# Kernel optimization log

Hardware: AMD Instinct MI355X
Metric: run time of the kernel (lower is better)

The kernel has to match this reference:

```python
import jax, jax.numpy as jnp
import numpy as np


def _conv3x3(x, w):
    # NCHW input, OIHW weight, stride 1, padding 1 (SAME for 3x3)
    return jax.lax.conv_general_dilated(
        x, w, window_strides=(1, 1), padding=((1, 1), (1, 1)),
        dimension_numbers=('NCHW', 'OIHW', 'NCHW'))


def _conv1x1(x, w):
    return jax.lax.conv_general_dilated(
        x, w, window_strides=(1, 1), padding=((0, 0), (0, 0)),
        dimension_numbers=('NCHW', 'OIHW', 'NCHW'))


def setup_inputs() -> dict:
    key = jax.random.key(0)
    k_x, k_w1, k_w2, k_wm = jax.random.split(key, 4)
    N, C, H, W = 16, 256, 64, 64
    fan = C * 9
    x = jax.random.normal(k_x, (N, C, H, W), dtype=jnp.float32)
    w1 = jax.random.normal(k_w1, (C, C, 3, 3), dtype=jnp.float32) * (2.0 / fan) ** 0.5
    w2 = jax.random.normal(k_w2, (C, C, 3, 3), dtype=jnp.float32) * (2.0 / fan) ** 0.5
    w_mask = jax.random.normal(k_wm, (1, C, 1, 1), dtype=jnp.float32) * (1.0 / C) ** 0.5
    b_mask = jnp.zeros((1,), dtype=jnp.float32)
    return {'x': x, 'w1': w1, 'w2': w2, 'w_mask': w_mask, 'b_mask': b_mask}


def reference(x, w1, w2, w_mask, b_mask):
    # MaskUnit: 1x1 conv -> logits -> hard binary mask (straight-through estimator)
    logits = _conv1x1(x, w_mask) + b_mask[None, :, None, None]  # [N,1,H,W]
    hard = (logits > 0).astype(x.dtype)
    mask = logits + jax.lax.stop_gradient(hard - logits)        # std mask, binary in fwd
    # dilated mask: 3x3 max-pool (covers 3x3 receptive field of active outputs)
    mask_dilate = jax.lax.reduce_window(
        mask, -jnp.inf, jax.lax.max, (1, 1, 3, 3), (1, 1, 1, 1), 'SAME')
    # sparse branch: conv1 gated by dilated mask, conv2 gated by std mask
    h = jax.nn.relu(_conv3x3(x, w1) * mask_dilate)
    h = jax.nn.relu(_conv3x3(h, w2) * mask)
    # apply_mask + residual (mask binary -> h*mask == h already, kept for fidelity)
    out = x + h * mask
    return out
```

## Files before the change

kernel.cpp:

```cpp
#include <hip/hip_runtime.h>
#include <hip/hip_bf16.h>

#define C_ 256
#define H_ 64
#define W_ 64
#define N_ 16
#define HW_ 4096
#define IMG_ (C_ * HW_)
#define PADIMG_ (66 * 66 * 256)
#define WT_ELEMS_ (9 * 16 * 256 * 16)

typedef short bf16x8 __attribute__((ext_vector_type(8)));
typedef float f32x16 __attribute__((ext_vector_type(16)));

__device__ __forceinline__ unsigned short f2bf(float f) {
  __hip_bfloat16 h = __float2bfloat16(f);
  return *reinterpret_cast<unsigned short*>(&h);
}

__device__ __forceinline__ void gld_lds16(const void* g, void* l) {
  __builtin_amdgcn_global_load_lds(
      (const __attribute__((address_space(1))) void*)g,
      (__attribute__((address_space(3))) void*)l, 16, 0, 0);
}

__global__ __launch_bounds__(256) void xpadmask_kernel(
    const float* __restrict__ x, const float* __restrict__ wm,
    const float* __restrict__ bm, short* __restrict__ Xp,
    unsigned char* __restrict__ mask) {
  __shared__ unsigned short lds[64 * 260];
  __shared__ float wms[256];
  __shared__ double sums[4][64];
  const int h = blockIdx.x, img = blockIdx.y;
  const int tid = threadIdx.x;
  const int wv = tid >> 6, wl = tid & 63;
  wms[tid] = wm[tid];
  __syncthreads();
  const float* xi = x + (size_t)img * IMG_ + h * 64;
  double a0 = 0.0, a1 = 0.0, a2 = 0.0, a3 = 0.0;
#pragma unroll 4
  for (int i = 0; i < 16; ++i) {
#pragma unroll
    for (int u = 0; u < 4; ++u) {
      int c = (i * 4 + u) * 4 + wv;
      float v = xi[(size_t)c * HW_ + wl];
      lds[wl * 260 + c] = f2bf(v);
      double p = (double)v * (double)wms[c];
      if (u == 0) a0 += p;
      else if (u == 1) a1 += p;
      else if (u == 2) a2 += p;
      else a3 += p;
    }
  }
  sums[wv][wl] = (a0 + a1) + (a2 + a3);
  __syncthreads();
  short* Xpi = Xp + (size_t)img * PADIMG_ + ((h + 1) * 66 + 1) * 256;
#pragma unroll
  for (int j = 0; j < 16; ++j) {
    int w = j * 4 + wv;
    int c4 = wl * 4;
    uint2 d = *(const uint2*)&lds[w * 260 + c4];
    *(uint2*)&Xpi[(size_t)w * 256 + c4] = d;
  }
  if (wv == 0) {
    double t = sums[0][wl] + sums[1][wl] + sums[2][wl] + sums[3][wl] +
               (double)bm[0];
    mask[img * HW_ + h * 64 + wl] = (t > 0.0) ? 1 : 0;
  }
}

__global__ __launch_bounds__(256) void wt_kernel(
    const float* __restrict__ w1, const float* __restrict__ w2,
    short* __restrict__ Wt1, short* __restrict__ Wt2) {
  const int k = blockIdx.x, c = threadIdx.x;
  const float* src = blockIdx.y ? w2 : w1;
  short* dst = blockIdx.y ? Wt2 : Wt1;
  const float* s = src + ((size_t)k * 256 + c) * 9;
  const int kc = c >> 4, ce = c & 15;
#pragma unroll
  for (int t = 0; t < 9; ++t)
    dst[(((size_t)t * 16 + kc) * 256 + k) * 16 + ce] = (short)f2bf(s[t]);
}

__global__ __launch_bounds__(128) void halo_zero(short* __restrict__ Xp,
                                                 short* __restrict__ Hp) {
  int p = blockIdx.x;
  int r, c;
  if (p < 66) { r = 0; c = p; }
  else if (p < 132) { r = 65; c = p - 66; }
  else if (p < 196) { r = p - 131; c = 0; }
  else { r = p - 195; c = 65; }
  short* buf = blockIdx.z ? Hp : Xp;
  unsigned int* d = (unsigned int*)(buf + (size_t)blockIdx.y * PADIMG_ +
                                    (size_t)(r * 66 + c) * 256);
  d[threadIdx.x] = 0u;
}

#define BBUF 10560

__device__ __forceinline__ void stage_B(short* sm, int buf, const short* Xb,
                                        int ko, int wave, int lane) {
  short* Bd = sm + buf * BBUF;
#pragma unroll
  for (int q = 0; q < 3; ++q) {
    int n = wave + 8 * q;
    if (n > 21) n = 21;
    const int h = (n >= 11) ? 1 : 0;
    const int i = n - h * 11;
    const int row0 = (i < 10) ? i * 64 : 596;
    gld_lds16(Xb + (size_t)(row0 + lane) * 256 + ko + h * 8,
              Bd + h * 5280 + row0 * 8);
  }
}

template <int EPI>
__global__ __launch_bounds__(512, 4) void conv_mfma(
    const short* __restrict__ src, const short* __restrict__ Wt,
    const unsigned char* __restrict__ gate, const float* __restrict__ xres,
    short* __restrict__ dstH, float* __restrict__ dstF, int swz) {
  __shared__ __align__(16) short sm[3 * BBUF];

  const int tid = threadIdx.x;
  const int lane = tid & 63, wave = tid >> 6;
  const int ln31 = lane & 31, kh = lane >> 5;

  int bx, by, bz;
  {
    int d = blockIdx.x + 4 * (blockIdx.y + 8 * blockIdx.z);
    if (swz) {
      int k = d & 7, j = d >> 3;
      bx = j & 3;
      by = (j >> 2) & 7;
      bz = ((j >> 5) << 3) + k;
    } else {
      bx = blockIdx.x;
      by = blockIdx.y;
      bz = blockIdx.z;
    }
  }
  const int ch0 = bx * 64;
  const int h0 = by * 8;
  const int img = bz;

  const short* Xb = src + (size_t)img * PADIMG_ + (size_t)(h0 * 66) * 256;
  const short* WL = Wt + ((size_t)(ch0 + ln31)) * 16 + kh * 8;

  f32x16 acc[2][2];
#pragma unroll
  for (int i = 0; i < 2; ++i)
#pragma unroll
    for (int j = 0; j < 2; ++j)
#pragma unroll
      for (int e = 0; e < 16; ++e) acc[i][j][e] = 0.f;

  stage_B(sm, 0, Xb, 0, wave, lane);
  stage_B(sm, 1, Xb, 16, wave, lane);
  bf16x8 wc0 = *(const bf16x8*)(WL);
  bf16x8 wc1 = *(const bf16x8*)(WL + 512);
  asm volatile("s_waitcnt vmcnt(2)\n\ts_barrier" ::: "memory");

  int c0 = 0, c1 = 1, c2 = 2;
  for (int kk = 0; kk < 16; ++kk) {
    const short* Bth = sm + c0 * BBUF + kh * 5280 + (wave * 66 + ln31) * 8;
#pragma unroll
    for (int t = 0; t < 9; ++t) {
      const int ntkc = (t < 8) ? ((t + 1) * 16 + kk) : (kk + 1);
      bf16x8 na0 = *(const bf16x8*)(WL + (size_t)ntkc * 4096);
      bf16x8 na1 = *(const bf16x8*)(WL + (size_t)ntkc * 4096 + 512);
      const int dy = t / 3, dx = t % 3;
      bf16x8 b[2];
#pragma unroll
      for (int j = 0; j < 2; ++j)
        b[j] = *(const bf16x8*)(Bth + (dy * 66 + j * 32 + dx) * 8);
      __builtin_amdgcn_s_setprio(1);
#pragma unroll
      for (int j = 0; j < 2; ++j) {
        acc[0][j] = __builtin_amdgcn_mfma_f32_32x32x16_bf16(wc0, b[j],
                                                            acc[0][j], 0, 0, 0);
        acc[1][j] = __builtin_amdgcn_mfma_f32_32x32x16_bf16(wc1, b[j],
                                                            acc[1][j], 0, 0, 0);
      }
      __builtin_amdgcn_s_setprio(0);
      wc0 = na0;
      wc1 = na1;
    }
    if (kk < 14) stage_B(sm, c2, Xb, (kk + 2) * 16, wave, lane);
    if (kk < 15) asm volatile("s_barrier" ::: "memory");
    const int tmp = c0;
    c0 = c1;
    c1 = c2;
    c2 = tmp;
  }

  const int r = h0 + wave;
#pragma unroll
  for (int j = 0; j < 2; ++j) {
    const int col = j * 32 + ln31;
    const int pidx = r * 64 + col;
    unsigned int g;
    if (EPI == 0) {
      g = 0;
#pragma unroll
      for (int dy = -1; dy <= 1; ++dy) {
        const int rr = r + dy;
        if (rr < 0 || rr >= H_) continue;
#pragma unroll
        for (int dx = -1; dx <= 1; ++dx) {
          const int cc = col + dx;
          if (cc < 0 || cc >= W_) continue;
          g |= gate[img * HW_ + rr * W_ + cc];
        }
      }
    } else {
      g = gate[img * HW_ + pidx];
    }
#pragma unroll
    for (int i = 0; i < 2; ++i) {
      const f32x16 v = acc[i][j];
#pragma unroll
      for (int rg = 0; rg < 4; ++rg) {
        const int ch = ch0 + i * 32 + rg * 8 + kh * 4;
        float e0 = g ? fmaxf(v[rg * 4 + 0], 0.f) : 0.f;
        float e1 = g ? fmaxf(v[rg * 4 + 1], 0.f) : 0.f;
        float e2 = g ? fmaxf(v[rg * 4 + 2], 0.f) : 0.f;
        float e3 = g ? fmaxf(v[rg * 4 + 3], 0.f) : 0.f;
        if (EPI == 0) {
          uint2 u;
          u.x = (unsigned int)f2bf(e0) | ((unsigned int)f2bf(e1) << 16);
          u.y = (unsigned int)f2bf(e2) | ((unsigned int)f2bf(e3) << 16);
          short* dp = dstH + (size_t)img * PADIMG_ +
                      ((size_t)((r + 1) * 66 + (col + 1))) * 256 + ch;
          *(uint2*)dp = u;
        } else {
          size_t o = (size_t)img * IMG_ + (size_t)ch * HW_ + pidx;
          dstF[o] = xres[o] + e0;
          dstF[o + HW_] = xres[o + HW_] + e1;
          dstF[o + 2 * HW_] = xres[o + 2 * HW_] + e2;
          dstF[o + 3 * HW_] = xres[o + 3 * HW_] + e3;
        }
      }
    }
  }
}

extern "C" void kernel_launch(void* const* d_in, const int* in_sizes, int n_in,
                              void* d_out, int out_size, void* d_ws,
                              size_t ws_size, hipStream_t stream) {
  const float* x = (const float*)d_in[0];
  const float* w1 = (const float*)d_in[1];
  const float* w2 = (const float*)d_in[2];
  const float* wmask = (const float*)d_in[3];
  const float* bmask = (const float*)d_in[4];
  float* out = (float*)d_out;

  char* ws = (char*)d_ws;
  unsigned char* mask = (unsigned char*)ws;
  short* Wt1 = (short*)(ws + 65536);
  short* Wt2 = Wt1 + WT_ELEMS_;
  const size_t fixed = 65536 + 4 * (size_t)WT_ELEMS_;
  short* Xp = (short*)(ws + fixed);

  const size_t tailpad = 32768;
  const size_t per_img = 2 * (size_t)PADIMG_ * 2;
  int B = (ws_size > fixed + tailpad)
              ? (int)((ws_size - fixed - tailpad) / per_img) : 0;
  if (B > N_) B = N_;
  if (B < 1) B = 1;
  short* Hp = Xp + (size_t)B * PADIMG_;

  wt_kernel<<<dim3(256, 2), 256, 0, stream>>>(w1, w2, Wt1, Wt2);
  halo_zero<<<dim3(260, B, 2), 128, 0, stream>>>(Xp, Hp);

  for (int n0 = 0; n0 < N_; n0 += B) {
    const int nb = (N_ - n0 < B) ? (N_ - n0) : B;
    const int swz = (nb % 8 == 0) ? 1 : 0;
    xpadmask_kernel<<<dim3(64, nb), 256, 0, stream>>>(
        x + (size_t)n0 * IMG_, wmask, bmask, Xp, mask + n0 * HW_);
    conv_mfma<0><<<dim3(4, 8, nb), 512, 0, stream>>>(
        Xp, Wt1, mask + n0 * HW_, nullptr, Hp, nullptr, swz);
    conv_mfma<1><<<dim3(4, 8, nb), 512, 0, stream>>>(
        Hp, Wt2, mask + n0 * HW_, x + (size_t)n0 * IMG_, nullptr,
        out + (size_t)n0 * IMG_, swz);
  }
}
```

Baseline: 314.6 us.

## Stage conv weights through LDS with double-buffered global_load_lds

The weight fragments used to come straight from global memory into registers for each tap. They are now staged into LDS alongside the input tile using async global-to-LDS loads. The input buffering drops from three buffers to two, and the next chunk's loads are issued at the start of each K-step so they overlap the MFMA work. Operand reads from LDS are software-pipelined one tap ahead. The cost is a full vmcnt(0) wait and barrier every K-step with only two buffers, and more LDS per block, which may cut occupancy.

Measured after the change: 289.2 us. -8.1%, faster.

```diff
diff --git a/kernel.cpp b/kernel.cpp
--- a/kernel.cpp
+++ b/kernel.cpp
@@ -97,19 +97,31 @@
 }
 
 #define BBUF 10560
-
-__device__ __forceinline__ void stage_B(short* sm, int buf, const short* Xb,
-                                        int ko, int wave, int lane) {
+#define WOFF 21120
+#define WBUF 9216
+
+__device__ __forceinline__ void stage_BW(short* sm, int buf, const short* Xb,
+                                         const short* Wg, int ch0, int kc,
+                                         int wave, int lane) {
   short* Bd = sm + buf * BBUF;
-#pragma unroll
-  for (int q = 0; q < 3; ++q) {
-    int n = wave + 8 * q;
-    if (n > 21) n = 21;
-    const int h = (n >= 11) ? 1 : 0;
-    const int i = n - h * 11;
-    const int row0 = (i < 10) ? i * 64 : 596;
-    gld_lds16(Xb + (size_t)(row0 + lane) * 256 + ko + h * 8,
-              Bd + h * 5280 + row0 * 8);
+  short* Wd = sm + WOFF + buf * WBUF;
+  const int ko = kc * 16;
+#pragma unroll
+  for (int q = 0; q < 5; ++q) {
+    const int n = wave + 8 * q;
+    if (n < 22) {
+      const int h = (n >= 11) ? 1 : 0;
+      const int i = n - h * 11;
+      const int row0 = (i < 10) ? i * 64 : 596;
+      gld_lds16(Xb + (size_t)(row0 + lane) * 256 + ko + h * 8,
+                Bd + h * 5280 + row0 * 8);
+    } else {
+      const int m = n - 22;
+      const int t = m >> 1, ih = m & 1;
+      gld_lds16(Wg + (((size_t)t * 16 + kc) * 256 + ch0 + ih * 32 +
+                      (lane & 31)) * 16 + (lane >> 5) * 8,
+                Wd + (t * 2 + ih) * 512);
+    }
   }
 }
 
@@ -118,7 +130,7 @@
     const short* __restrict__ src, const short* __restrict__ Wt,
     const unsigned char* __restrict__ gate, const float* __restrict__ xres,
     short* __restrict__ dstH, float* __restrict__ dstF, int swz) {
-  __shared__ __align__(16) short sm[3 * BBUF];
+  __shared__ __align__(16) short sm[2 * BBUF + 2 * WBUF];
 
   const int tid = threadIdx.x;
   const int lane = tid & 63, wave = tid >> 6;
@@ -143,7 +155,6 @@
   const int img = bz;
 
   const short* Xb = src + (size_t)img * PADIMG_ + (size_t)(h0 * 66) * 256;
-  const short* WL = Wt + ((size_t)(ch0 + ln31)) * 16 + kh * 8;
 
   f32x16 acc[2][2];
 #pragma unroll
@@ -153,43 +164,53 @@
 #pragma unroll
       for (int e = 0; e < 16; ++e) acc[i][j][e] = 0.f;
 
-  stage_B(sm, 0, Xb, 0, wave, lane);
-  stage_B(sm, 1, Xb, 16, wave, lane);
-  bf16x8 wc0 = *(const bf16x8*)(WL);
-  bf16x8 wc1 = *(const bf16x8*)(WL + 512);
-  asm volatile("s_waitcnt vmcnt(2)\n\ts_barrier" ::: "memory");
-
-  int c0 = 0, c1 = 1, c2 = 2;
+  stage_BW(sm, 0, Xb, Wt, ch0, 0, wave, lane);
+  asm volatile("s_waitcnt vmcnt(0)\n\ts_barrier" ::: "memory");
+
   for (int kk = 0; kk < 16; ++kk) {
-    const short* Bth = sm + c0 * BBUF + kh * 5280 + (wave * 66 + ln31) * 8;
+    const int cur = kk & 1;
+    if (kk < 15) stage_BW(sm, cur ^ 1, Xb, Wt, ch0, kk + 1, wave, lane);
+
+    const short* Bth = sm + cur * BBUF + kh * 5280 + (wave * 66 + ln31) * 8;
+    const short* Wth = sm + WOFF + cur * WBUF + (kh * 32 + ln31) * 8;
+
+    bf16x8 ac[2], bc[2], an[2], bn[2];
+#pragma unroll
+    for (int i = 0; i < 2; ++i)
+      ac[i] = *(const bf16x8*)(Wth + (0 * 2 + i) * 512);
+#pragma unroll
+    for (int j = 0; j < 2; ++j)
+      bc[j] = *(const bf16x8*)(Bth + (0 * 66 + j * 32 + 0) * 8);
+
 #pragma unroll
     for (int t = 0; t < 9; ++t) {
-      const int ntkc = (t < 8) ? ((t + 1) * 16 + kk) : (kk + 1);
-      bf16x8 na0 = *(const bf16x8*)(WL + (size_t)ntkc * 4096);
-      bf16x8 na1 = *(const bf16x8*)(WL + (size_t)ntkc * 4096 + 512);
-      const int dy = t / 3, dx = t % 3;
-      bf16x8 b[2];
-#pragma unroll
-      for (int j = 0; j < 2; ++j)
-        b[j] = *(const bf16x8*)(Bth + (dy * 66 + j * 32 + dx) * 8);
+      if (t < 8) {
+        const int dy = (t + 1) / 3, dx = (t + 1) % 3;
+#pragma unroll
+        for (int i = 0; i < 2; ++i)
+          an[i] = *(const bf16x8*)(Wth + ((t + 1) * 2 + i) * 512);
+#pragma unroll
+        for (int j = 0; j < 2; ++j)
+          bn[j] = *(const bf16x8*)(Bth + (dy * 66 + j * 32 + dx) * 8);
+      }
       __builtin_amdgcn_s_setprio(1);
 #pragma unroll
       for (int j = 0; j < 2; ++j) {
-        acc[0][j] = __builtin_amdgcn_mfma_f32_32x32x16_bf16(wc0, b[j],
+        acc[0][j] = __builtin_amdgcn_mfma_f32_32x32x16_bf16(ac[0], bc[j],
                                                             acc[0][j], 0, 0, 0);
-        acc[1][j] = __builtin_amdgcn_mfma_f32_32x32x16_bf16(wc1, b[j],
+        acc[1][j] = __builtin_amdgcn_mfma_f32_32x32x16_bf16(ac[1], bc[j],
                                                             acc[1][j], 0, 0, 0);
       }
       __builtin_amdgcn_s_setprio(0);
-      wc0 = na0;
-      wc1 = na1;
-    }
-    if (kk < 14) stage_B(sm, c2, Xb, (kk + 2) * 16, wave, lane);
-    if (kk < 15) asm volatile("s_barrier" ::: "memory");
-    const int tmp = c0;
-    c0 = c1;
-    c1 = c2;
-    c2 = tmp;
+      if (t < 8) {
+#pragma unroll
+        for (int i = 0; i < 2; ++i) ac[i] = an[i];
+#pragma unroll
+        for (int j = 0; j < 2; ++j) bc[j] = bn[j];
+      }
+    }
+    if (kk < 15)
+      asm volatile("s_waitcnt vmcnt(0)\n\ts_barrier" ::: "memory");
   }
 
   const int r = h0 + wave;
```
